# Performance work log

Hardware: AMD Instinct MI355X
Metric: run time of the kernel (lower is better)

The kernel has to match this reference:

```python
import jax, jax.numpy as jnp
import numpy as np

HIDDEN = 100
INPUT = 4


def setup_inputs() -> dict:
    key = jax.random.key(0)
    k_x, k_len, k_wi, k_wh, k_bi, k_bh = jax.random.split(key, 6)
    N, T = 4096, 256
    x = jax.random.normal(k_x, (N, T, INPUT), dtype=jnp.float32)
    lengths = jax.random.randint(k_len, (N,), 1, T + 1, dtype=jnp.int32)
    # PyTorch LSTM params: weight_ih [4H, I], weight_hh [4H, H] (uniform(-0.05,0.05)
    # per the module's init), biases [4H]. Gate order: i, f, g, o.
    s = 1.0 / np.sqrt(HIDDEN)
    w_ih = jax.random.uniform(k_wi, (4 * HIDDEN, INPUT), minval=-s, maxval=s, dtype=jnp.float32)
    w_hh = jax.random.uniform(k_wh, (4 * HIDDEN, HIDDEN), minval=-0.05, maxval=0.05, dtype=jnp.float32)
    b_ih = jax.random.uniform(k_bi, (4 * HIDDEN,), minval=-s, maxval=s, dtype=jnp.float32)
    b_hh = jax.random.uniform(k_bh, (4 * HIDDEN,), minval=-s, maxval=s, dtype=jnp.float32)
    return {"long_ttf": x, "w_ih": w_ih, "w_hh": w_hh, "b_ih": b_ih, "b_hh": b_hh, "lengths": lengths}


def _lstm_last(x, w_ih, w_hh, b_ih, b_hh, lengths):
    # x: [N, T, I]; returns h at step (length-1) per sequence -> [N, H]
    N, T, _ = x.shape
    xs = jnp.swapaxes(x, 0, 1)  # [T, N, I]
    # mask[t, n] = t < lengths[n]; freeze (h, c) once a sequence has ended,
    # so the final carry equals the output at its last valid step.
    mask = (jnp.arange(T, dtype=jnp.int32)[:, None] < lengths[None, :])[:, :, None]  # [T, N, 1]
    bias = b_ih + b_hh

    def step(carry, inp):
        h, c = carry
        xt, m = inp
        gates = xt @ w_ih.T + h @ w_hh.T + bias  # [N, 4H]
        i = jax.nn.sigmoid(gates[:, 0 * HIDDEN:1 * HIDDEN])
        f = jax.nn.sigmoid(gates[:, 1 * HIDDEN:2 * HIDDEN])
        g = jnp.tanh(gates[:, 2 * HIDDEN:3 * HIDDEN])
        o = jax.nn.sigmoid(gates[:, 3 * HIDDEN:4 * HIDDEN])
        c_new = f * c + i * g
        h_new = o * jnp.tanh(c_new)
        h = jnp.where(m, h_new, h)
        c = jnp.where(m, c_new, c)
        return (h, c), None

    h0 = jnp.zeros((N, HIDDEN), dtype=x.dtype)
    c0 = jnp.zeros((N, HIDDEN), dtype=x.dtype)
    (h, _), _ = jax.lax.scan(step, (h0, c0), (xs, mask))
    return h


def reference(long_ttf, w_ih, w_hh, b_ih, b_hh, lengths):
    return _lstm_last(long_ttf, w_ih, w_hh, b_ih, b_hh, lengths)
```

## Files before the change

### kernel.cpp

```cpp
#include <hip/hip_runtime.h>

#define HID    100
#define GATES  400
#define INP    4
#define TMAX   256
#define SB     16
#define ULD    136
#define NTH    1024
#define NTILES 25

typedef _Float16 half8 __attribute__((ext_vector_type(8)));
typedef float    f32x4 __attribute__((ext_vector_type(4)));

#define L2E  1.442695040888963f
#define L2E2 2.885390081777927f

__device__ __forceinline__ float fexp2(float x) { return __builtin_amdgcn_exp2f(x); }
__device__ __forceinline__ float frcp(float x)  { return __builtin_amdgcn_rcpf(x); }

__global__ __launch_bounds__(NTH) void lstm_persist(
    const float* __restrict__ xg,
    const float* __restrict__ w_ih,
    const float* __restrict__ w_hh,
    const float* __restrict__ b_ih,
    const float* __restrict__ b_hh,
    const int*   __restrict__ lens,
    float* __restrict__ out)
{
    __shared__ _Float16 u_lds[2][SB * ULD];
    __shared__ int len_s[SB];
    __shared__ int maxlen_s;

    const int tid  = threadIdx.x;
    const int wave = tid >> 6;
    const int lane = tid & 63;
    const int l15  = lane & 15;
    const int l4   = lane >> 4;
    const int seq0 = blockIdx.x * SB;

    if (tid < SB) len_s[tid] = lens[seq0 + tid];
    {
        _Float16* u0 = &u_lds[0][0];
        for (int i = tid; i < 2 * SB * ULD; i += NTH) {
            int col = i % ULD;
            u0[i] = (col == (HID + INP)) ? (_Float16)1.f : (_Float16)0.f;
        }
    }

    half8 afrag[2][4];
    int   tn[2];
    tn[0] = wave;
    tn[1] = (wave + 16 < NTILES) ? wave + 16 : NTILES;
    #pragma unroll
    for (int i = 0; i < 2; ++i) {
        int n = tn[i];
        if (n < NTILES) {
            int p  = n * 16 + l15;
            int ty = p & 3;
            int q  = p >> 2;
            int unit = 25 * (q & 3) + (q >> 2);
            int grow = ty * HID + unit;
            float scale = (ty == 2) ? L2E2 : -L2E;
            #pragma unroll
            for (int c = 0; c < 4; ++c) {
                half8 v;
                #pragma unroll
                for (int j = 0; j < 8; ++j) {
                    int k = c * 32 + l4 * 8 + j;
                    float w;
                    if (k < HID)             w = w_hh[grow * HID + k];
                    else if (k < HID + INP)  w = w_ih[grow * INP + (k - HID)];
                    else if (k == HID + INP) w = b_ih[grow] + b_hh[grow];
                    else                     w = 0.f;
                    v[j] = (_Float16)(scale * w);
                }
                afrag[i][c] = v;
            }
        }
    }

    __syncthreads();
    if (tid == 0) {
        int m = 0;
        for (int s = 0; s < SB; ++s) m = m > len_s[s] ? m : len_s[s];
        maxlen_s = m;
    }

    float xv1 = 0.f, xv2 = 0.f;
    if (tid >= NTH - 64) {
        int idx = tid - (NTH - 64);
        int s = idx >> 2, ch = idx & 3;
        const float* xs = xg + (size_t)(seq0 + s) * TMAX * INP + ch;
        u_lds[0][s * ULD + HID + ch] = (_Float16)xs[0];
        xv1 = xs[INP];
        xv2 = xs[2 * INP];
    }
    float creg[2] = {};
    __syncthreads();

    if (wave & 1) __builtin_amdgcn_s_setprio(1);

    const int maxlen = maxlen_s;
    const int mylen  = len_s[l15];
    const _Float16* ub0 = &u_lds[0][l15 * ULD + l4 * 8];
    const _Float16* ub1 = &u_lds[1][l15 * ULD + l4 * 8];

    for (int t = 0; t < maxlen; ++t) {
        const _Float16* ub = (t & 1) ? ub1 : ub0;
        _Float16* ubn = (t & 1) ? &u_lds[0][0] : &u_lds[1][0];

        half8 bfr[4];
        #pragma unroll
        for (int c = 0; c < 4; ++c)
            bfr[c] = *(const half8*)(ub + c * 32);

        if (tid >= NTH - 64) {
            int idx = tid - (NTH - 64);
            int s = idx >> 2, ch = idx & 3;
            ubn[s * ULD + HID + ch] = (_Float16)xv1;
            xv1 = xv2;
            int tt = t + 3;
            xv2 = (tt < TMAX) ? xg[((size_t)(seq0 + s) * TMAX + tt) * INP + ch] : 0.f;
        }

        #pragma unroll
        for (int i = 0; i < 2; ++i) {
            if (tn[i] < NTILES) {
                f32x4 acc = {0.f, 0.f, 0.f, 0.f};
                #pragma unroll
                for (int c = 0; c < 4; ++c)
                    acc = __builtin_amdgcn_mfma_f32_16x16x32_f16(afrag[i][c], bfr[c], acc, 0, 0, 0);
                if (t < mylen) {
                    float e_i = fexp2(acc[0]);
                    float e_f = fexp2(acc[1]);
                    float e_g = fexp2(acc[2]);
                    float e_o = fexp2(acc[3]);
                    float tg  = 1.f + e_g;
                    float d1  = __builtin_fmaf(e_i, tg, tg);
                    float r1  = frcp(d1);
                    float ig  = __builtin_fmaf(e_g, r1, -r1);
                    float r2  = frcp(1.f + e_f);
                    float cn  = __builtin_fmaf(r2, creg[i], ig);
                    float e_c = fexp2(fminf(L2E2 * cn, 60.f));
                    float t3  = 1.f + e_c;
                    float d3  = __builtin_fmaf(e_o, t3, t3);
                    float r3  = frcp(d3);
                    float hn  = __builtin_fmaf(e_c, r3, -r3);
                    creg[i] = cn;
                    int unit = 25 * l4 + tn[i];
                    ubn[l15 * ULD + unit] = (_Float16)hn;
                    if (t == mylen - 1)
                        out[(size_t)(seq0 + l15) * HID + unit] = hn;
                }
            }
        }
        asm volatile("s_waitcnt lgkmcnt(0)" ::: "memory");
        __builtin_amdgcn_s_barrier();
    }
}

extern "C" void kernel_launch(void* const* d_in, const int* in_sizes, int n_in,
                              void* d_out, int out_size, void* d_ws, size_t ws_size,
                              hipStream_t stream) {
    const float* xg   = (const float*)d_in[0];
    const float* w_ih = (const float*)d_in[1];
    const float* w_hh = (const float*)d_in[2];
    const float* b_ih = (const float*)d_in[3];
    const float* b_hh = (const float*)d_in[4];
    const int*   lens = (const int*)d_in[5];
    float* out = (float*)d_out;
    const int N = in_sizes[5];
    lstm_persist<<<dim3(N / SB), NTH, 0, stream>>>(xg, w_ih, w_hh, b_ih, b_hh, lens, out);
}
```

Measured before the change: 164.4 us.

## Sort sequences by length and pack 8 per block for balanced early exit

Adds a single-block counting-sort kernel that orders sequence indices by descending length. The LSTM kernel then gathers 8 length-sorted sequences per 512-thread block instead of 16 contiguous ones. Each block's loop bound (max length) now sits close to every member's length, which cuts steps wasted on already-finished sequences. In exchange it runs an extra serial launch, uses only half of each 16-wide MFMA column tile, gives each wave up to four tiles, and doubles the block count.

```diff
diff --git a/kernel.cpp b/kernel.cpp
--- a/kernel.cpp
+++ b/kernel.cpp
@@ -1,12 +1,11 @@
 #include <hip/hip_runtime.h>
 
 #define HID    100
-#define GATES  400
 #define INP    4
 #define TMAX   256
-#define SB     16
+#define SBR    8
 #define ULD    136
-#define NTH    1024
+#define NTH    512
 #define NTILES 25
 
 typedef _Float16 half8 __attribute__((ext_vector_type(8)));
@@ -18,17 +17,41 @@
 __device__ __forceinline__ float fexp2(float x) { return __builtin_amdgcn_exp2f(x); }
 __device__ __forceinline__ float frcp(float x)  { return __builtin_amdgcn_rcpf(x); }
 
-__global__ __launch_bounds__(NTH) void lstm_persist(
+__global__ __launch_bounds__(1024) void sort_by_len(const int* __restrict__ lens,
+                                                    int* __restrict__ perm, int N) {
+    __shared__ int hist[256];
+    __shared__ int base[256];
+    __shared__ int cnt[256];
+    const int tid = threadIdx.x;
+    for (int i = tid; i < 256; i += 1024) { hist[i] = 0; cnt[i] = 0; }
+    __syncthreads();
+    for (int i = tid; i < N; i += 1024)
+        atomicAdd(&hist[256 - lens[i]], 1);
+    __syncthreads();
+    if (tid == 0) {
+        int acc = 0;
+        for (int k = 0; k < 256; ++k) { base[k] = acc; acc += hist[k]; }
+    }
+    __syncthreads();
+    for (int i = tid; i < N; i += 1024) {
+        int key = 256 - lens[i];
+        perm[base[key] + atomicAdd(&cnt[key], 1)] = i;
+    }
+}
+
+__global__ __launch_bounds__(NTH, 4) void lstm_persist(
     const float* __restrict__ xg,
     const float* __restrict__ w_ih,
     const float* __restrict__ w_hh,
     const float* __restrict__ b_ih,
     const float* __restrict__ b_hh,
     const int*   __restrict__ lens,
+    const int*   __restrict__ perm,
     float* __restrict__ out)
 {
-    __shared__ _Float16 u_lds[2][SB * ULD];
-    __shared__ int len_s[SB];
+    __shared__ _Float16 u_lds[2][16 * ULD];
+    __shared__ int len_s[SBR];
+    __shared__ int sid_s[SBR];
     __shared__ int maxlen_s;
 
     const int tid  = threadIdx.x;
@@ -36,23 +59,27 @@
     const int lane = tid & 63;
     const int l15  = lane & 15;
     const int l4   = lane >> 4;
-    const int seq0 = blockIdx.x * SB;
-
-    if (tid < SB) len_s[tid] = lens[seq0 + tid];
+    const int g0   = blockIdx.x * SBR;
+
+    if (tid < SBR) {
+        int sid = perm[g0 + tid];
+        sid_s[tid] = sid;
+        len_s[tid] = lens[sid];
+    }
     {
         _Float16* u0 = &u_lds[0][0];
-        for (int i = tid; i < 2 * SB * ULD; i += NTH) {
+        for (int i = tid; i < 2 * 16 * ULD; i += NTH) {
             int col = i % ULD;
             u0[i] = (col == (HID + INP)) ? (_Float16)1.f : (_Float16)0.f;
         }
     }
 
-    half8 afrag[2][4];
-    int   tn[2];
-    tn[0] = wave;
-    tn[1] = (wave + 16 < NTILES) ? wave + 16 : NTILES;
+    half8 afrag[4][4];
+    int   tn[4];
+    tn[0] = wave; tn[1] = wave + 8; tn[2] = wave + 16;
+    tn[3] = (wave == 6) ? 24 : NTILES;
     #pragma unroll
-    for (int i = 0; i < 2; ++i) {
+    for (int i = 0; i < 4; ++i) {
         int n = tn[i];
         if (n < NTILES) {
             int p  = n * 16 + l15;
@@ -82,26 +109,28 @@
     __syncthreads();
     if (tid == 0) {
         int m = 0;
-        for (int s = 0; s < SB; ++s) m = m > len_s[s] ? m : len_s[s];
+        for (int s = 0; s < SBR; ++s) m = m > len_s[s] ? m : len_s[s];
         maxlen_s = m;
     }
 
     float xv1 = 0.f, xv2 = 0.f;
-    if (tid >= NTH - 64) {
-        int idx = tid - (NTH - 64);
+    const float* xs = nullptr;
+    if (tid >= NTH - 32) {
+        int idx = tid - (NTH - 32);
         int s = idx >> 2, ch = idx & 3;
-        const float* xs = xg + (size_t)(seq0 + s) * TMAX * INP + ch;
+        xs = xg + (size_t)sid_s[s] * TMAX * INP + ch;
         u_lds[0][s * ULD + HID + ch] = (_Float16)xs[0];
         xv1 = xs[INP];
         xv2 = xs[2 * INP];
     }
-    float creg[2] = {};
+    float creg[4] = {};
     __syncthreads();
 
     if (wave & 1) __builtin_amdgcn_s_setprio(1);
 
     const int maxlen = maxlen_s;
-    const int mylen  = len_s[l15];
+    const int mylen  = (l15 < SBR) ? len_s[l15] : 0;
+    const int myseq  = (l15 < SBR) ? sid_s[l15] : 0;
     const _Float16* ub0 = &u_lds[0][l15 * ULD + l4 * 8];
     const _Float16* ub1 = &u_lds[1][l15 * ULD + l4 * 8];
 
@@ -114,17 +143,17 @@
         for (int c = 0; c < 4; ++c)
             bfr[c] = *(const half8*)(ub + c * 32);
 
-        if (tid >= NTH - 64) {
-            int idx = tid - (NTH - 64);
+        if (tid >= NTH - 32) {
+            int idx = tid - (NTH - 32);
             int s = idx >> 2, ch = idx & 3;
             ubn[s * ULD + HID + ch] = (_Float16)xv1;
             xv1 = xv2;
             int tt = t + 3;
-            xv2 = (tt < TMAX) ? xg[((size_t)(seq0 + s) * TMAX + tt) * INP + ch] : 0.f;
+            xv2 = (tt < TMAX) ? xs[(size_t)tt * INP] : 0.f;
         }
 
         #pragma unroll
-        for (int i = 0; i < 2; ++i) {
+        for (int i = 0; i < 4; ++i) {
             if (tn[i] < NTILES) {
                 f32x4 acc = {0.f, 0.f, 0.f, 0.f};
                 #pragma unroll
@@ -150,7 +179,7 @@
                     int unit = 25 * l4 + tn[i];
                     ubn[l15 * ULD + unit] = (_Float16)hn;
                     if (t == mylen - 1)
-                        out[(size_t)(seq0 + l15) * HID + unit] = hn;
+                        out[(size_t)myseq * HID + unit] = hn;
                 }
             }
         }
@@ -170,5 +199,8 @@
     const int*   lens = (const int*)d_in[5];
     float* out = (float*)d_out;
     const int N = in_sizes[5];
-    lstm_persist<<<dim3(N / SB), NTH, 0, stream>>>(xg, w_ih, w_hh, b_ih, b_hh, lens, out);
+    int* perm = (int*)d_ws;
+    sort_by_len<<<1, 1024, 0, stream>>>(lens, perm, N);
+    lstm_persist<<<dim3(N / SBR), NTH, 0, stream>>>(xg, w_ih, w_hh, b_ih, b_hh,
+                                                    lens, perm, out);
 }
```

Result: slower. 206.5 us (+25.6%).

## Remap hidden-unit ownership so paired tiles write packed half2 to LDS

Applied to the files above, without the earlier changes.

Changes the mapping of MFMA tile rows to hidden units so that the two tiles a wave owns produce adjacent hidden indices. This lets each lane store both results as one packed half2 LDS write. It also issues both tiles' MFMAs before either activation chain, and replaces the two reciprocals for the input and forget gates with a single shared reciprocal. The x-prefetch address is reused from a saved pointer. The intent is fewer LDS stores and better overlap between MFMA and transcendental work on the serial per-timestep critical path, at the cost of a more intricate unit permutation that must stay consistent between weights and outputs.

```diff
diff --git a/kernel.cpp b/kernel.cpp
--- a/kernel.cpp
+++ b/kernel.cpp
@@ -1,7 +1,6 @@
 #include <hip/hip_runtime.h>
 
 #define HID    100
-#define GATES  400
 #define INP    4
 #define TMAX   256
 #define SB     16
@@ -9,14 +8,24 @@
 #define NTH    1024
 #define NTILES 25
 
-typedef _Float16 half8 __attribute__((ext_vector_type(8)));
-typedef float    f32x4 __attribute__((ext_vector_type(4)));
+typedef _Float16 half8  __attribute__((ext_vector_type(8)));
+typedef _Float16 half2v __attribute__((ext_vector_type(2)));
+typedef float    f32x4  __attribute__((ext_vector_type(4)));
 
 #define L2E  1.442695040888963f
 #define L2E2 2.885390081777927f
 
 __device__ __forceinline__ float fexp2(float x) { return __builtin_amdgcn_exp2f(x); }
 __device__ __forceinline__ float frcp(float x)  { return __builtin_amdgcn_rcpf(x); }
+
+__device__ __forceinline__ int pos_for(int n, int g) {
+    int base = 25 * g;
+    int e = base + (base & 1);
+    if (n < 9)   return e + 2 * n;
+    if (n >= 16) return e + 2 * (n - 16) + 1;
+    if (base & 1) return (n == 9) ? base : base + 19 + (n - 10);
+    return base + 18 + (n - 9);
+}
 
 __global__ __launch_bounds__(NTH) void lstm_persist(
     const float* __restrict__ xg,
@@ -55,10 +64,8 @@
     for (int i = 0; i < 2; ++i) {
         int n = tn[i];
         if (n < NTILES) {
-            int p  = n * 16 + l15;
-            int ty = p & 3;
-            int q  = p >> 2;
-            int unit = 25 * (q & 3) + (q >> 2);
+            int ty   = l15 & 3;
+            int unit = pos_for(n, l15 >> 2);
             int grow = ty * HID + unit;
             float scale = (ty == 2) ? L2E2 : -L2E;
             #pragma unroll
@@ -87,10 +94,11 @@
     }
 
     float xv1 = 0.f, xv2 = 0.f;
+    const float* xs = nullptr;
     if (tid >= NTH - 64) {
         int idx = tid - (NTH - 64);
         int s = idx >> 2, ch = idx & 3;
-        const float* xs = xg + (size_t)(seq0 + s) * TMAX * INP + ch;
+        xs = xg + (size_t)(seq0 + s) * TMAX * INP + ch;
         u_lds[0][s * ULD + HID + ch] = (_Float16)xs[0];
         xv1 = xs[INP];
         xv2 = xs[2 * INP];
@@ -99,6 +107,10 @@
     __syncthreads();
 
     if (wave & 1) __builtin_amdgcn_s_setprio(1);
+
+    const bool has2 = (wave < 9);
+    const int  pos0 = pos_for(tn[0], l4);
+    const int  pos1 = has2 ? pos_for(tn[1], l4) : 0;
 
     const int maxlen = maxlen_s;
     const int mylen  = len_s[l15];
@@ -120,38 +132,71 @@
             ubn[s * ULD + HID + ch] = (_Float16)xv1;
             xv1 = xv2;
             int tt = t + 3;
-            xv2 = (tt < TMAX) ? xg[((size_t)(seq0 + s) * TMAX + tt) * INP + ch] : 0.f;
-        }
-
+            xv2 = (tt < TMAX) ? xs[(size_t)tt * INP] : 0.f;
+        }
+
+        f32x4 acc0 = {0.f, 0.f, 0.f, 0.f};
         #pragma unroll
-        for (int i = 0; i < 2; ++i) {
-            if (tn[i] < NTILES) {
-                f32x4 acc = {0.f, 0.f, 0.f, 0.f};
-                #pragma unroll
-                for (int c = 0; c < 4; ++c)
-                    acc = __builtin_amdgcn_mfma_f32_16x16x32_f16(afrag[i][c], bfr[c], acc, 0, 0, 0);
-                if (t < mylen) {
-                    float e_i = fexp2(acc[0]);
-                    float e_f = fexp2(acc[1]);
-                    float e_g = fexp2(acc[2]);
-                    float e_o = fexp2(acc[3]);
-                    float tg  = 1.f + e_g;
-                    float d1  = __builtin_fmaf(e_i, tg, tg);
-                    float r1  = frcp(d1);
-                    float ig  = __builtin_fmaf(e_g, r1, -r1);
-                    float r2  = frcp(1.f + e_f);
-                    float cn  = __builtin_fmaf(r2, creg[i], ig);
-                    float e_c = fexp2(fminf(L2E2 * cn, 60.f));
-                    float t3  = 1.f + e_c;
-                    float d3  = __builtin_fmaf(e_o, t3, t3);
-                    float r3  = frcp(d3);
-                    float hn  = __builtin_fmaf(e_c, r3, -r3);
-                    creg[i] = cn;
-                    int unit = 25 * l4 + tn[i];
-                    ubn[l15 * ULD + unit] = (_Float16)hn;
-                    if (t == mylen - 1)
-                        out[(size_t)(seq0 + l15) * HID + unit] = hn;
-                }
+        for (int c = 0; c < 4; ++c)
+            acc0 = __builtin_amdgcn_mfma_f32_16x16x32_f16(afrag[0][c], bfr[c], acc0, 0, 0, 0);
+        f32x4 acc1 = {0.f, 0.f, 0.f, 0.f};
+        if (has2) {
+            #pragma unroll
+            for (int c = 0; c < 4; ++c)
+                acc1 = __builtin_amdgcn_mfma_f32_16x16x32_f16(afrag[1][c], bfr[c], acc1, 0, 0, 0);
+        }
+
+        if (t < mylen) {
+            float e_i = fexp2(acc0[0]);
+            float e_f = fexp2(acc0[1]);
+            float e_g = fexp2(acc0[2]);
+            float e_o = fexp2(acc0[3]);
+            float tg  = 1.f + e_g;
+            float df  = 1.f + e_f;
+            float d1  = __builtin_fmaf(e_i, tg, tg);
+            float r12 = frcp(d1 * df);
+            float r1  = df * r12;
+            float fm  = d1 * r12;
+            float ig  = __builtin_fmaf(e_g, r1, -r1);
+            float cn  = __builtin_fmaf(fm, creg[0], ig);
+            float e_c = fexp2(fminf(L2E2 * cn, 60.f));
+            float t3  = 1.f + e_c;
+            float d3  = __builtin_fmaf(e_o, t3, t3);
+            float r3  = frcp(d3);
+            float hn0 = __builtin_fmaf(e_c, r3, -r3);
+            creg[0] = cn;
+
+            float hn1 = 0.f;
+            if (has2) {
+                float f_i = fexp2(acc1[0]);
+                float f_f = fexp2(acc1[1]);
+                float f_g = fexp2(acc1[2]);
+                float f_o = fexp2(acc1[3]);
+                float ug  = 1.f + f_g;
+                float uf  = 1.f + f_f;
+                float u1  = __builtin_fmaf(f_i, ug, ug);
+                float s12 = frcp(u1 * uf);
+                float s1  = uf * s12;
+                float um  = u1 * s12;
+                float jg  = __builtin_fmaf(f_g, s1, -s1);
+                float dn  = __builtin_fmaf(um, creg[1], jg);
+                float f_c = fexp2(fminf(L2E2 * dn, 60.f));
+                float u3  = 1.f + f_c;
+                float w3  = __builtin_fmaf(f_o, u3, u3);
+                float s3  = frcp(w3);
+                hn1 = __builtin_fmaf(f_c, s3, -s3);
+                creg[1] = dn;
+            }
+
+            if (has2) {
+                half2v pk = {(_Float16)hn0, (_Float16)hn1};
+                *(half2v*)(ubn + l15 * ULD + pos0) = pk;
+            } else {
+                ubn[l15 * ULD + pos0] = (_Float16)hn0;
+            }
+            if (t == mylen - 1) {
+                out[(size_t)(seq0 + l15) * HID + pos0] = hn0;
+                if (has2) out[(size_t)(seq0 + l15) * HID + pos1] = hn1;
             }
         }
         asm volatile("s_waitcnt lgkmcnt(0)" ::: "memory");
```

Measured after the change: 178.4 us. 1.09x slower.
